# Kernel optimization log

Measured on AMD Instinct MI355X. Metric: run time of the kernel, lower is better.

## Reference

```python
import jax, jax.numpy as jnp
import numpy as np

HEADS = 12
WH = WW = 7
N = WH * WW  # 49 tokens per window
NW = 64      # windows per image (mask groups)


def _relative_position_index():
    ch, cw = np.meshgrid(np.arange(WH), np.arange(WW), indexing='ij')
    coords = np.stack([ch, cw]).reshape(2, -1)  # [2, N]
    rel = coords[:, :, None] - coords[:, None, :]  # [2, N, N]
    rel = rel.transpose(1, 2, 0)
    rel[:, :, 0] += WH - 1
    rel[:, :, 1] += WW - 1
    rel[:, :, 0] *= 2 * WW - 1
    return rel.sum(-1).astype(np.int32)  # [N, N]


def setup_inputs() -> dict:
    key = jax.random.key(0)
    ks = jax.random.split(key, 6)
    B, C = 4096, 384
    x = jax.random.normal(ks[0], (B, N, C), dtype=jnp.float32)
    mask = jnp.where(jax.random.uniform(ks[1], (NW, N, N)) > 0.5, 0.0, -100.0).astype(jnp.float32)
    W_qkv = jax.random.normal(ks[2], (C, 3 * C), dtype=jnp.float32) * 0.02
    b_qkv = jnp.zeros((3 * C,), dtype=jnp.float32)
    W_out = jax.random.normal(ks[3], (C, C), dtype=jnp.float32) * 0.02
    b_out = jnp.zeros((C,), dtype=jnp.float32)
    rpb_table = jax.random.normal(ks[4], ((2 * WH - 1) * (2 * WW - 1), HEADS), dtype=jnp.float32) * 0.01
    rel_index = jnp.asarray(_relative_position_index())
    return {"x": x, "mask": mask, "W_qkv": W_qkv, "b_qkv": b_qkv,
            "W_out": W_out, "b_out": b_out, "rpb_table": rpb_table,
            "rel_index": rel_index}


def reference(x, mask, W_qkv, b_qkv, W_out, b_out, rpb_table, rel_index):
    B, n, C = x.shape
    hd = C // HEADS
    scale = hd ** (-0.5)
    qkv = x @ W_qkv + b_qkv                      # [B, n, 3C]
    q, k, v = jnp.split(qkv, 3, axis=2)
    def heads(t):
        return t.reshape(B, n, HEADS, hd).transpose(0, 2, 1, 3)  # b h n d
    q = heads(q) * scale
    k = heads(k)
    v = heads(v)
    attn = jnp.einsum('bhmc,bhnc->bhmn', q, k)   # [B, h, n, n]
    bias = rpb_table[rel_index.reshape(-1)].reshape(n, n, HEADS).transpose(2, 0, 1)
    attn = attn + bias[None]
    nw = mask.shape[0]
    attn = attn.reshape(B // nw, nw, HEADS, n, n) + mask[None, :, None]
    attn = attn.reshape(B, HEADS, n, n)
    attn = jax.nn.softmax(attn, axis=3)
    out = jnp.einsum('bhmn,bhnc->bhmc', attn, v)  # [B, h, n, d]
    out = out.transpose(0, 2, 1, 3).reshape(B, n, C)
    return out @ W_out + b_out
```

## Files before the change

kernel.cpp:

```cpp
#include <hip/hip_runtime.h>

#define NTOK 49
#define CDIM 384
#define HEADS 12
#define HD 32
#define NWIN 64
#define NQKV 1152
#define SCALE 0.17677669529663687f

typedef __attribute__((ext_vector_type(8))) __bf16 bf16x8;
typedef __attribute__((ext_vector_type(4))) float f32x4;

#define OFF_WQKVT   0ull
#define OFF_WOUTT   884736ull
#define OFF_ADDEND  1179648ull
#define OFF_QKVB    8555520ull
#define OFF_ATTNOUT 470977536ull
#define OFF_XB      OFF_ATTNOUT

#define TSIZE 77070336ull

__device__ __forceinline__ void async_copy16(__bf16* lds_dst, const __bf16* g_src) {
    __builtin_amdgcn_global_load_lds(
        (const __attribute__((address_space(1))) void*)g_src,
        (__attribute__((address_space(3))) void*)lds_dst,
        16, 0, 0);
}


__global__ void prep_weights(const float* __restrict__ Wqkv, const float* __restrict__ Wout,
                             __bf16* __restrict__ WqkvT, __bf16* __restrict__ WoutT) {
    int idx = blockIdx.x * 256 + threadIdx.x;
    if (idx < NQKV * CDIM) {
        int n = idx / CDIM, k = idx % CDIM;
        WqkvT[idx] = (__bf16)Wqkv[(size_t)k * NQKV + n];
    }
    if (idx < CDIM * CDIM) {
        int n = idx / CDIM, k = idx % CDIM;
        WoutT[idx] = (__bf16)Wout[(size_t)k * CDIM + n];
    }
}

__global__ void prep_addend(const float* __restrict__ rpb, const int* __restrict__ rel,
                            const float* __restrict__ mask, float* __restrict__ addend) {
    int idx = blockIdx.x * 256 + threadIdx.x;
    if (idx >= NWIN * HEADS * NTOK * NTOK) return;
    int mn = idx % (NTOK * NTOK);
    int h  = (idx / (NTOK * NTOK)) % HEADS;
    int w  = idx / (NTOK * NTOK * HEADS);
    addend[idx] = rpb[rel[mn] * HEADS + h] + mask[(size_t)w * NTOK * NTOK + mn];
}

__global__ __launch_bounds__(256) void prep_xb(const float* __restrict__ x,
                                               __bf16* __restrict__ xb, int total8) {
    int stride = gridDim.x * 256;
    for (int i = blockIdx.x * 256 + threadIdx.x; i < total8; i += stride) {
        float4 a = reinterpret_cast<const float4*>(x)[i * 2];
        float4 b = reinterpret_cast<const float4*>(x)[i * 2 + 1];
        union { __bf16 h[8]; uint4 u; } t;
        t.h[0] = (__bf16)a.x; t.h[1] = (__bf16)a.y; t.h[2] = (__bf16)a.z; t.h[3] = (__bf16)a.w;
        t.h[4] = (__bf16)b.x; t.h[5] = (__bf16)b.y; t.h[6] = (__bf16)b.z; t.h[7] = (__bf16)b.w;
        reinterpret_cast<uint4*>(xb)[i] = t.u;
    }
}


__global__ __launch_bounds__(256, 3) void gemm_qkv(
    const __bf16* __restrict__ xb, const __bf16* __restrict__ WqkvT,
    const float* __restrict__ bqkv, __bf16* __restrict__ qkvb)
{
    __shared__ __attribute__((aligned(16))) __bf16 smem[16384];
    __bf16* As = smem;
    __bf16* Bs = smem + 8192;

    const int cpx  = 14112 >> 3;
    const int lid  = (blockIdx.x & 7) * cpx + (blockIdx.x >> 3);
    const int mblk = lid / 9, nblk = lid % 9;
    const int n0  = nblk * 128;
    const int bm0 = mblk * 128;

    const int tid = threadIdx.x;
    const int wave = tid >> 6, lane = tid & 63;
    const int l15 = lane & 15, l4 = lane >> 4;
    const int wr = wave >> 1, wc = wave & 1;

    f32x4 acc[4][4] = {};

    for (int k0 = 0; k0 < CDIM; k0 += 64) {
#pragma unroll
        for (int j = 0; j < 4; ++j) {
            int c = wave * 4 + j;
            int mt = c >> 1, kk = c & 1;
            const __bf16* sa = xb + (size_t)(bm0 + mt * 16 + l15) * CDIM + k0 + kk * 32 + l4 * 8;
            async_copy16(&As[c * 512], sa);
            const __bf16* sb = WqkvT + (size_t)(n0 + mt * 16 + l15) * CDIM + k0 + kk * 32 + l4 * 8;
            async_copy16(&Bs[c * 512], sb);
        }
        __syncthreads();

#pragma unroll
        for (int kk = 0; kk < 2; ++kk) {
            bf16x8 af[4], bf[4];
#pragma unroll
            for (int mi = 0; mi < 4; ++mi)
                af[mi] = *reinterpret_cast<const bf16x8*>(&As[((wr * 4 + mi) * 2 + kk) * 512 + lane * 8]);
#pragma unroll
            for (int ni = 0; ni < 4; ++ni)
                bf[ni] = *reinterpret_cast<const bf16x8*>(&Bs[((wc * 4 + ni) * 2 + kk) * 512 + lane * 8]);
#pragma unroll
            for (int mi = 0; mi < 4; ++mi)
#pragma unroll
                for (int ni = 0; ni < 4; ++ni)
                    acc[mi][ni] = __builtin_amdgcn_mfma_f32_16x16x32_bf16(af[mi], bf[ni], acc[mi][ni], 0, 0, 0);
        }
        __syncthreads();
    }

    const float scl = (n0 < CDIM) ? SCALE : 1.0f;
    float bias[4];
#pragma unroll
    for (int ni = 0; ni < 4; ++ni)
        bias[ni] = bqkv[n0 + wc * 64 + ni * 16 + l15];

    __bf16* Cs = smem;
#pragma unroll
    for (int mi = 0; mi < 4; ++mi)
#pragma unroll
        for (int ni = 0; ni < 4; ++ni)
#pragma unroll
            for (int r = 0; r < 4; ++r) {
                int row = wr * 64 + mi * 16 + l4 * 4 + r;
                int col = wc * 64 + ni * 16 + l15;
                int byte = (row * 256 + col * 2) ^ (((row >> 2) & 3) << 5);
                *reinterpret_cast<__bf16*>(reinterpret_cast<char*>(Cs) + byte) =
                    (__bf16)((acc[mi][ni][r] + bias[ni]) * scl);
            }
    __syncthreads();

    const int which = n0 / CDIM;
    const int h0    = (n0 % CDIM) >> 5;
    __bf16* tbase = qkvb + (size_t)which * TSIZE;
#pragma unroll
    for (int it = 0; it < 8; ++it) {
        int idx = it * 4096 + tid * 16;
        int row = idx >> 8, bcol = idx & 255;
        int sb = (row * 256 + bcol) ^ (((row >> 2) & 3) << 5);
        uint4 v = *reinterpret_cast<const uint4*>(reinterpret_cast<const char*>(Cs) + sb);
        int grow = bm0 + row;
        int b = grow / NTOK, tok = grow - b * NTOK;
        int col = bcol >> 1;
        int h = h0 + (col >> 5), d = col & 31;
        *reinterpret_cast<uint4*>(&tbase[(((size_t)b * HEADS + h) * NTOK + tok) * HD + d]) = v;
    }
}


__global__ __launch_bounds__(256) void attn(
    const __bf16* __restrict__ qkvb, const float* __restrict__ addend,
    __bf16* __restrict__ attnout)
{
    __shared__ __attribute__((aligned(16))) __bf16 vt[4][32 * 64];
    __shared__ __attribute__((aligned(16))) __bf16 ps[4][2][64][8];
    const int b = blockIdx.x;
    const int tid = threadIdx.x;
    const int wave = tid >> 6, lane = tid & 63;
    const int l15 = lane & 15, l4 = lane >> 4;
    const int h = blockIdx.y * 4 + wave;
    const int w = b & (NWIN - 1);

    const size_t hoff = (((size_t)b * HEADS + h) * NTOK) * HD;
    const __bf16* qb = qkvb + hoff;
    const __bf16* kb = qkvb + TSIZE + hoff;
    const __bf16* vb = qkvb + 2 * TSIZE + hoff;

    {
        const int tokb = lane >> 2;
        const int c8   = (lane & 3) * 8;
#pragma unroll
        for (int i = 0; i < 4; ++i) {
            int tok = i * 16 + tokb;
            bf16x8 vv = *reinterpret_cast<const bf16x8*>(vb + (size_t)tok * HD + c8);
#pragma unroll
            for (int j = 0; j < 8; ++j) {
                int d = c8 + j;
                vt[wave][d * 64 + (tok ^ ((d & 7) << 3))] = vv[j];
            }
        }
    }

    bf16x8 kf[4];
#pragma unroll
    for (int nt = 0; nt < 4; ++nt)
        kf[nt] = *reinterpret_cast<const bf16x8*>(kb + (size_t)(nt * 16 + l15) * HD + l4 * 8);

    const float* add_h = addend + (size_t)(w * HEADS + h) * (NTOK * NTOK);

    for (int mt = 0; mt < 4; ++mt) {
        bf16x8 qf = *reinterpret_cast<const bf16x8*>(qb + (size_t)(mt * 16 + l15) * HD + l4 * 8);
        f32x4 s[4];
#pragma unroll
        for (int nt = 0; nt < 4; ++nt) {
            f32x4 z = {};
            s[nt] = __builtin_amdgcn_mfma_f32_16x16x32_bf16(qf, kf[nt], z, 0, 0, 0);
        }

#pragma unroll
        for (int r = 0; r < 4; ++r) {
            int m = mt * 16 + l4 * 4 + r;
            float vals[4];
#pragma unroll
            for (int nt = 0; nt < 4; ++nt) {
                int n = nt * 16 + l15;
                float sv = s[nt][r];
                if (n < NTOK) {
                    if (m < NTOK) sv += add_h[m * NTOK + n];
                } else {
                    sv = -1e30f;
                }
                vals[nt] = sv;
            }
            float mx = fmaxf(fmaxf(vals[0], vals[1]), fmaxf(vals[2], vals[3]));
            mx = fmaxf(mx, __shfl_xor(mx, 1));
            mx = fmaxf(mx, __shfl_xor(mx, 2));
            mx = fmaxf(mx, __shfl_xor(mx, 4));
            mx = fmaxf(mx, __shfl_xor(mx, 8));
            float e0 = __expf(vals[0] - mx);
            float e1 = __expf(vals[1] - mx);
            float e2 = __expf(vals[2] - mx);
            float e3 = __expf(vals[3] - mx);
            float sum = (e0 + e1) + (e2 + e3);
            sum += __shfl_xor(sum, 1);
            sum += __shfl_xor(sum, 2);
            sum += __shfl_xor(sum, 4);
            sum += __shfl_xor(sum, 8);
            float inv = 1.0f / sum;
            float ev[4] = {e0, e1, e2, e3};
#pragma unroll
            for (int nt = 0; nt < 4; ++nt) {
                int lp = (l4 * 4 + r) + 16 * ((nt & 1) * 2 + (l15 >> 3));
                ps[wave][nt >> 1][lp][l15 & 7] = (__bf16)(ev[nt] * inv);
            }
        }

        f32x4 o[2] = {};
#pragma unroll
        for (int kb2 = 0; kb2 < 2; ++kb2) {
            bf16x8 ap = *reinterpret_cast<const bf16x8*>(&ps[wave][kb2][lane][0]);
#pragma unroll
            for (int dt = 0; dt < 2; ++dt) {
                int d = dt * 16 + l15;
                bf16x8 bv = *reinterpret_cast<const bf16x8*>(
                    &vt[wave][d * 64 + ((kb2 * 32 + l4 * 8) ^ ((l15 & 7) << 3))]);
                o[dt] = __builtin_amdgcn_mfma_f32_16x16x32_bf16(ap, bv, o[dt], 0, 0, 0);
            }
        }
#pragma unroll
        for (int dt = 0; dt < 2; ++dt) {
            int col = h * HD + dt * 16 + l15;
#pragma unroll
            for (int r = 0; r < 4; ++r) {
                int tok = mt * 16 + l4 * 4 + r;
                if (tok < NTOK)
                    attnout[((size_t)b * NTOK + tok) * CDIM + col] = (__bf16)o[dt][r];
            }
        }
    }
}


__global__ __launch_bounds__(256, 3) void out_proj(
    const __bf16* __restrict__ A, const __bf16* __restrict__ WoutT,
    const float* __restrict__ bout, float* __restrict__ out)
{
    __shared__ __attribute__((aligned(16))) __bf16 as[4 * 12 * 512];
    const int blk = blockIdx.x, tid = threadIdx.x;
    const int wave = tid >> 6, lane = tid & 63;
    const int l15 = lane & 15, l4 = lane >> 4;

    const __bf16* Ab = A + (size_t)blk * 64 * CDIM;
    for (int i = tid; i < 64 * CDIM / 8; i += 256) {
        int4 ld = reinterpret_cast<const int4*>(Ab)[i];
        int e = i * 8;
        int row = e / CDIM, c = e % CDIM;
        int mt = row >> 4, kb = c >> 5;
        int lp = (row & 15) + 16 * ((c & 31) >> 3);
        int slot = lp ^ (kb & 7);
        *reinterpret_cast<int4*>(&as[((mt * 12 + kb) * 64 + slot) * 8]) = ld;
    }
    __syncthreads();

    f32x4 acc[6][4] = {};
    for (int kb = 0; kb < 12; ++kb) {
        int slot = lane ^ (kb & 7);
        bf16x8 af[4];
#pragma unroll
        for (int mt = 0; mt < 4; ++mt)
            af[mt] = *reinterpret_cast<const bf16x8*>(&as[((mt * 12 + kb) * 64 + slot) * 8]);
#pragma unroll
        for (int j = 0; j < 6; ++j) {
            int col = (wave * 6 + j) * 16 + l15;
            bf16x8 bf = *reinterpret_cast<const bf16x8*>(WoutT + (size_t)col * CDIM + kb * 32 + l4 * 8);
#pragma unroll
            for (int mt = 0; mt < 4; ++mt)
                acc[j][mt] = __builtin_amdgcn_mfma_f32_16x16x32_bf16(af[mt], bf, acc[j][mt], 0, 0, 0);
        }
    }
#pragma unroll
    for (int j = 0; j < 6; ++j) {
        int col = (wave * 6 + j) * 16 + l15;
        float bias = bout[col];
#pragma unroll
        for (int mt = 0; mt < 4; ++mt) {
#pragma unroll
            for (int r = 0; r < 4; ++r) {
                size_t row = (size_t)blk * 64 + mt * 16 + l4 * 4 + r;
                out[row * CDIM + col] = acc[j][mt][r] + bias;
            }
        }
    }
}


extern "C" void kernel_launch(void* const* d_in, const int* in_sizes, int n_in,
                              void* d_out, int out_size, void* d_ws, size_t ws_size,
                              hipStream_t stream) {
    (void)n_in; (void)out_size; (void)ws_size;
    const float* x    = (const float*)d_in[0];
    const float* mask = (const float*)d_in[1];
    const float* Wqkv = (const float*)d_in[2];
    const float* bqkv = (const float*)d_in[3];
    const float* Wout = (const float*)d_in[4];
    const float* bout = (const float*)d_in[5];
    const float* rpb  = (const float*)d_in[6];
    const int*   rel  = (const int*)d_in[7];

    const int B = in_sizes[0] / (NTOK * CDIM);
    const int M = B * NTOK;

    char* ws = (char*)d_ws;
    __bf16* WqkvT   = (__bf16*)(ws + OFF_WQKVT);
    __bf16* WoutT   = (__bf16*)(ws + OFF_WOUTT);
    float*  addend  = (float*)(ws + OFF_ADDEND);
    __bf16* qkvb    = (__bf16*)(ws + OFF_QKVB);
    __bf16* xb      = (__bf16*)(ws + OFF_XB);
    __bf16* attnout = (__bf16*)(ws + OFF_ATTNOUT);
    float*  out     = (float*)d_out;

    prep_weights<<<(NQKV * CDIM + 255) / 256, 256, 0, stream>>>(Wqkv, Wout, WqkvT, WoutT);
    prep_addend<<<(NWIN * HEADS * NTOK * NTOK + 255) / 256, 256, 0, stream>>>(rpb, rel, mask, addend);
    prep_xb<<<2048, 256, 0, stream>>>(x, xb, M * CDIM / 8);
    gemm_qkv<<<(M / 128) * (NQKV / 128), 256, 0, stream>>>(xb, WqkvT, bqkv, qkvb);
    attn<<<dim3(B, 3), 256, 0, stream>>>(qkvb, addend, attnout);
    out_proj<<<M / 64, 256, 0, stream>>>(attnout, WoutT, bout, out);
}
```

Before: 927.3 us.

## Precompute bias and mask in MFMA fragment layout for vectorized loads

The combined per-window, per-head addend table is replaced by two separate tables, relative-position bias per head and mask per window. Both are stored in the MFMA accumulator fragment order, so each lane does coalesced 16-byte loads instead of scattered scalar loads guarded by bounds checks. This shrinks the prep table from about 7 MB to about 1.2 MB, which should fit better in cache, at the cost of one extra add per score. The QKV GEMM launch bound also changes from 3 to 4 waves-per-block occupancy, which may increase register pressure.

Result: faster. 892.0 us (-3.8%).

```diff
diff --git a/kernel.cpp b/kernel.cpp
--- a/kernel.cpp
+++ b/kernel.cpp
@@ -13,7 +13,8 @@
 
 #define OFF_WQKVT   0ull
 #define OFF_WOUTT   884736ull
-#define OFF_ADDEND  1179648ull
+#define OFF_RPBF    1179648ull
+#define OFF_MASKF   1376256ull
 #define OFF_QKVB    8555520ull
 #define OFF_ATTNOUT 470977536ull
 #define OFF_XB      OFF_ATTNOUT
@@ -41,14 +42,22 @@
     }
 }
 
-__global__ void prep_addend(const float* __restrict__ rpb, const int* __restrict__ rel,
-                            const float* __restrict__ mask, float* __restrict__ addend) {
+__global__ void prep_frag(const float* __restrict__ rpb, const int* __restrict__ rel,
+                          const float* __restrict__ mask,
+                          float* __restrict__ rpbF, float* __restrict__ maskF) {
     int idx = blockIdx.x * 256 + threadIdx.x;
-    if (idx >= NWIN * HEADS * NTOK * NTOK) return;
-    int mn = idx % (NTOK * NTOK);
-    int h  = (idx / (NTOK * NTOK)) % HEADS;
-    int w  = idx / (NTOK * NTOK * HEADS);
-    addend[idx] = rpb[rel[mn] * HEADS + h] + mask[(size_t)w * NTOK * NTOK + mn];
+    if (idx < 49152) {
+        int r = idx & 3, lane = (idx >> 2) & 63, nt = (idx >> 8) & 3, mt = (idx >> 10) & 3, h = idx >> 12;
+        int m = mt * 16 + ((lane >> 4) << 2) + r, n = nt * 16 + (lane & 15);
+        rpbF[idx] = (m < NTOK && n < NTOK) ? rpb[rel[m * NTOK + n] * HEADS + h] : 0.f;
+    } else {
+        int i2 = idx - 49152;
+        if (i2 < 262144) {
+            int r = i2 & 3, lane = (i2 >> 2) & 63, nt = (i2 >> 8) & 3, mt = (i2 >> 10) & 3, w = i2 >> 12;
+            int m = mt * 16 + ((lane >> 4) << 2) + r, n = nt * 16 + (lane & 15);
+            maskF[i2] = (m < NTOK && n < NTOK) ? mask[(size_t)w * NTOK * NTOK + m * NTOK + n] : 0.f;
+        }
+    }
 }
 
 __global__ __launch_bounds__(256) void prep_xb(const float* __restrict__ x,
@@ -65,7 +74,7 @@
 }
 
 
-__global__ __launch_bounds__(256, 3) void gemm_qkv(
+__global__ __launch_bounds__(256, 4) void gemm_qkv(
     const __bf16* __restrict__ xb, const __bf16* __restrict__ WqkvT,
     const float* __restrict__ bqkv, __bf16* __restrict__ qkvb)
 {
@@ -156,8 +165,8 @@
 
 
 __global__ __launch_bounds__(256) void attn(
-    const __bf16* __restrict__ qkvb, const float* __restrict__ addend,
-    __bf16* __restrict__ attnout)
+    const __bf16* __restrict__ qkvb, const float* __restrict__ rpbF,
+    const float* __restrict__ maskF, __bf16* __restrict__ attnout)
 {
     __shared__ __attribute__((aligned(16))) __bf16 vt[4][32 * 64];
     __shared__ __attribute__((aligned(16))) __bf16 ps[4][2][64][8];
@@ -172,6 +181,8 @@
     const __bf16* qb = qkvb + hoff;
     const __bf16* kb = qkvb + TSIZE + hoff;
     const __bf16* vb = qkvb + 2 * TSIZE + hoff;
+    const f32x4* rpbF4  = reinterpret_cast<const f32x4*>(rpbF);
+    const f32x4* maskF4 = reinterpret_cast<const f32x4*>(maskF);
 
     {
         const int tokb = lane >> 2;
@@ -193,10 +204,16 @@
     for (int nt = 0; nt < 4; ++nt)
         kf[nt] = *reinterpret_cast<const bf16x8*>(kb + (size_t)(nt * 16 + l15) * HD + l4 * 8);
 
-    const float* add_h = addend + (size_t)(w * HEADS + h) * (NTOK * NTOK);
-
     for (int mt = 0; mt < 4; ++mt) {
         bf16x8 qf = *reinterpret_cast<const bf16x8*>(qb + (size_t)(mt * 16 + l15) * HD + l4 * 8);
+
+        f32x4 rb[4], mb[4];
+#pragma unroll
+        for (int nt = 0; nt < 4; ++nt) {
+            rb[nt] = rpbF4[((h * 4 + mt) * 4 + nt) * 64 + lane];
+            mb[nt] = maskF4[((w * 4 + mt) * 4 + nt) * 64 + lane];
+        }
+
         f32x4 s[4];
 #pragma unroll
         for (int nt = 0; nt < 4; ++nt) {
@@ -206,18 +223,11 @@
 
 #pragma unroll
         for (int r = 0; r < 4; ++r) {
-            int m = mt * 16 + l4 * 4 + r;
             float vals[4];
 #pragma unroll
             for (int nt = 0; nt < 4; ++nt) {
                 int n = nt * 16 + l15;
-                float sv = s[nt][r];
-                if (n < NTOK) {
-                    if (m < NTOK) sv += add_h[m * NTOK + n];
-                } else {
-                    sv = -1e30f;
-                }
-                vals[nt] = sv;
+                vals[nt] = (n < NTOK) ? (s[nt][r] + rb[nt][r] + mb[nt][r]) : -1e30f;
             }
             float mx = fmaxf(fmaxf(vals[0], vals[1]), fmaxf(vals[2], vals[3]));
             mx = fmaxf(mx, __shfl_xor(mx, 1));
@@ -340,16 +350,17 @@
     char* ws = (char*)d_ws;
     __bf16* WqkvT   = (__bf16*)(ws + OFF_WQKVT);
     __bf16* WoutT   = (__bf16*)(ws + OFF_WOUTT);
-    float*  addend  = (float*)(ws + OFF_ADDEND);
+    float*  rpbF    = (float*)(ws + OFF_RPBF);
+    float*  maskF   = (float*)(ws + OFF_MASKF);
     __bf16* qkvb    = (__bf16*)(ws + OFF_QKVB);
     __bf16* xb      = (__bf16*)(ws + OFF_XB);
     __bf16* attnout = (__bf16*)(ws + OFF_ATTNOUT);
     float*  out     = (float*)d_out;
 
     prep_weights<<<(NQKV * CDIM + 255) / 256, 256, 0, stream>>>(Wqkv, Wout, WqkvT, WoutT);
-    prep_addend<<<(NWIN * HEADS * NTOK * NTOK + 255) / 256, 256, 0, stream>>>(rpb, rel, mask, addend);
+    prep_frag<<<(49152 + 262144) / 256, 256, 0, stream>>>(rpb, rel, mask, rpbF, maskF);
     prep_xb<<<2048, 256, 0, stream>>>(x, xb, M * CDIM / 8);
     gemm_qkv<<<(M / 128) * (NQKV / 128), 256, 0, stream>>>(xb, WqkvT, bqkv, qkvb);
-    attn<<<dim3(B, 3), 256, 0, stream>>>(qkvb, addend, attnout);
+    attn<<<dim3(B, 3), 256, 0, stream>>>(qkvb, rpbF, maskF, attnout);
     out_proj<<<M / 64, 256, 0, stream>>>(attnout, WoutT, bout, out);
 }
```
